# Optimization experiments

Measured on AMD Instinct MI355X. Metric: run time of the kernel, lower is better.

The kernel has to match this reference:

```python
import jax, jax.numpy as jnp
import numpy as np

B, S, D, H = 2, 2048, 1024, 16
DK = D // H


def setup_inputs() -> dict:
    key = jax.random.key(0)
    ks = jax.random.split(key, 8)
    xavier = lambda k, shape: jax.random.uniform(k, shape, jnp.float32, -1.0, 1.0) * np.sqrt(6.0 / (shape[0] + shape[1]))
    return {
        "query": jax.random.normal(ks[0], (B, S, D), jnp.float32),
        "key": jax.random.normal(ks[1], (B, S, D), jnp.float32),
        "value": jax.random.normal(ks[2], (B, S, D), jnp.float32),
        # causal mask: True above the diagonal -> masked out
        "mask": jnp.broadcast_to(jnp.triu(jnp.ones((S, S), bool), k=1), (B, S, S)),
        "w_q": xavier(ks[3], (D, D)),  # torch Linear weight [out, in]
        "w_k": xavier(ks[4], (D, D)),
        "w_v": xavier(ks[5], (D, D)),
        "w_o": xavier(ks[6], (D, D)),
        "b_o": jnp.zeros((D,), jnp.float32),
    }


def reference(query, key, value, mask, w_q, w_k, w_v, w_o, b_o):
    b, sq, d = query.shape
    sk = key.shape[1]
    # projections (torch Linear: x @ W.T)
    Q = (query @ w_q.T).reshape(b, sq, H, DK).transpose(0, 2, 1, 3)  # [B,H,Sq,DK]
    K = (key @ w_k.T).reshape(b, sk, H, DK).transpose(0, 2, 1, 3)
    V = (value @ w_v.T).reshape(b, sk, H, DK).transpose(0, 2, 1, 3)
    scores = jnp.einsum('bhqd,bhkd->bhqk', Q, K) / np.sqrt(DK)
    scores = jnp.where(mask[:, None, :, :], jnp.float32(-1e9), scores)
    attn = jax.nn.softmax(scores, axis=-1)  # dropout is identity in eval
    out = jnp.einsum('bhqk,bhkd->bhqd', attn, V)
    out = out.transpose(0, 2, 1, 3).reshape(b, sq, d)
    return out @ w_o.T + b_o
```

## Files before the change

kernel.cpp:

```cpp
#include <hip/hip_runtime.h>
#include <hip/hip_bf16.h>
#include <stdint.h>


typedef __attribute__((ext_vector_type(4))) float  f32x4;
typedef __attribute__((ext_vector_type(4))) int    i32x4;
typedef __attribute__((ext_vector_type(8))) __bf16 bf16x8;
typedef __attribute__((ext_vector_type(4))) __bf16 bf16x4;
typedef __attribute__((ext_vector_type(2))) __bf16 bf16x2;

#define MFMA16(a, b, c) __builtin_amdgcn_mfma_f32_16x16x32_bf16((a), (b), (c), 0, 0, 0)

__device__ __forceinline__ void async16(const void* g, void* lds) {
  __builtin_amdgcn_global_load_lds(
      (const __attribute__((address_space(1))) uint32_t*)g,
      (__attribute__((address_space(3))) uint32_t*)lds,
      16, 0, 0);
}

__device__ __forceinline__ bf16x8 lds_swz_read(const __bf16* base, int row, int cchunk) {
  const int sw = cchunk ^ (row & 7);
  return *(const bf16x8*)((const char*)base + row * 128 + sw * 16);
}

__global__ void detect_dtype(const uint16_t* __restrict__ w, int* __restrict__ flag) {
  __shared__ int s;
  if (threadIdx.x == 0) s = 0;
  __syncthreads();
  int big = 0;
  for (int i = threadIdx.x; i < 8192; i += 256) {
    uint32_t u = ((uint32_t)w[i]) << 16;
    float f;
    __builtin_memcpy(&f, &u, 4);
    if (fabsf(f) > 1.0f) big = 1;
  }
  if (big) atomicOr(&s, 1);
  __syncthreads();
  if (threadIdx.x == 0) *flag = s;
}

struct CvtArgs { const void* src[8]; void* dst[8]; int n[8]; };

__global__ __launch_bounds__(256)
void convert_all(CvtArgs a, const int* __restrict__ flagp) {
  if (*flagp == 0) return;
  const int t = blockIdx.y;
  const int n = a.n[t];
  const int i0 = (blockIdx.x * 256 + threadIdx.x) * 8;
  if (i0 >= n) return;
  const float* s = (const float*)a.src[t];
  __bf16* d = (__bf16*)a.dst[t];
  bf16x8 v;
#pragma unroll
  for (int j = 0; j < 8; ++j) v[j] = (__bf16)s[i0 + j];
  *(bf16x8*)(d + i0) = v;
}

struct GemmArgs {
  const __bf16* A[3];    const __bf16* W[3];
  const __bf16* Acvt[3]; const __bf16* Wcvt[3];
  void* C[3]; float scale[3];
  const __bf16* bias; const __bf16* biascvt;
  const int* flagp; int mode;
};

__global__ __launch_bounds__(256, 3)
void gemm_nt(GemmArgs ga)
{
  constexpr int K = 1024;
  __shared__ __align__(16) __bf16 smem[16384];

  const int id = blockIdx.x + (blockIdx.y << 3) + (blockIdx.z << 8);
  const int mb = (id & 7) * 4 + ((id >> 3) & 3);
  const int rest = id >> 5;
  const int nb = rest & 7;
  const int z = rest >> 3;

  const int f = *ga.flagp;
  const __bf16* __restrict__ A = f ? ga.Acvt[z] : ga.A[z];
  const __bf16* __restrict__ W = f ? ga.Wcvt[z] : ga.W[z];
  void* __restrict__ C = ga.C[z];
  const float scale = ga.scale[z];
  const int mode = ga.mode;

  const int tid = threadIdx.x;
  const int lane = tid & 63;
  const int wave = tid >> 6;
  const int l15 = lane & 15;
  const int quad = lane >> 4;
  const int bm = mb * 128;
  const int bn = nb * 128;
  const int wm = (wave >> 1) * 64;
  const int wn = (wave & 1) * 64;

  auto stage = [&](int kt, int buf) {
    const int k0 = kt * 32;
    __bf16* As = smem + buf * 8192;
    __bf16* Bs = As + 4096;
#pragma unroll
    for (int r = 0; r < 2; ++r) {
      const int chunk = r * 256 + wave * 64 + lane;
      const int row = chunk >> 2, c = chunk & 3;
      async16(A + (size_t)(bm + row) * K + k0 + c * 8, As + (r * 256 + wave * 64) * 8);
      async16(W + (size_t)(bn + row) * K + k0 + c * 8, Bs + (r * 256 + wave * 64) * 8);
    }
  };

  f32x4 acc[4][4];
#pragma unroll
  for (int mi = 0; mi < 4; ++mi)
#pragma unroll
    for (int ni = 0; ni < 4; ++ni) {
      f32x4 zz = {0.f, 0.f, 0.f, 0.f};
      acc[mi][ni] = zz;
    }

  stage(0, 0);
  __syncthreads();

  for (int kt = 0; kt < K / 32; ++kt) {
    const int cur = kt & 1;
    const __bf16* As = smem + cur * 8192;
    const __bf16* Bs = As + 4096;

    bf16x8 af[4];
    bf16x8 bfr[4];
#pragma unroll
    for (int mi = 0; mi < 4; ++mi)
      af[mi] = *(const bf16x8*)(As + (wm + mi * 16 + l15) * 32 + quad * 8);
#pragma unroll
    for (int ni = 0; ni < 4; ++ni)
      bfr[ni] = *(const bf16x8*)(Bs + (wn + ni * 16 + l15) * 32 + quad * 8);

    if (kt + 1 < K / 32) stage(kt + 1, cur ^ 1);

#pragma unroll
    for (int mi = 0; mi < 4; ++mi)
#pragma unroll
      for (int ni = 0; ni < 4; ++ni)
        acc[mi][ni] = MFMA16(af[mi], bfr[ni], acc[mi][ni]);

    __syncthreads();
  }

  float bv[4] = {0.f, 0.f, 0.f, 0.f};
  if (mode == 1) {
    const __bf16* bias = f ? ga.biascvt : ga.bias;
#pragma unroll
    for (int ni = 0; ni < 4; ++ni) bv[ni] = (float)bias[bn + wn + ni * 16 + l15];
  }
  __bf16 (*Cs)[136] = (__bf16(*)[136])smem;

#pragma unroll
  for (int pass = 0; pass < 2; ++pass) {
    __syncthreads();
    if ((wave >> 1) == pass) {
#pragma unroll
      for (int mi = 0; mi < 4; ++mi)
#pragma unroll
        for (int ni = 0; ni < 4; ++ni)
#pragma unroll
          for (int r = 0; r < 4; ++r)
            Cs[mi * 16 + quad * 4 + r][wn + ni * 16 + l15] =
                (__bf16)(acc[mi][ni][r] * scale + bv[ni]);
    }
    __syncthreads();

    if (mode == 0) {
#pragma unroll
      for (int it = 0; it < 4; ++it) {
        const int cid = it * 256 + tid;
        const int off = cid & 7, seg = cid >> 3;
        const int hl = seg & 1, rowl = seg >> 1;
        f32x4 v = *(const f32x4*)(&Cs[rowl][hl * 64 + off * 8]);
        const int m = bm + pass * 64 + rowl;
        const int b = m >> 11, s = m & 2047;
        const int h = (bn >> 6) + hl;
        *(f32x4*)((__bf16*)C + ((size_t)(b * 16 + h) * 2048 + s) * 64 + off * 8) = v;
      }
    } else if (f) {
#pragma unroll
      for (int it = 0; it < 4; ++it) {
        const int cid = it * 256 + tid;
        const int off = cid & 15, rowl = cid >> 4;
        bf16x8 vb = *(const bf16x8*)(&Cs[rowl][off * 8]);
        const int m = bm + pass * 64 + rowl;
        float* dst = (float*)C + (size_t)m * 1024 + bn + off * 8;
        f32x4 lo, hi;
#pragma unroll
        for (int j = 0; j < 4; ++j) { lo[j] = (float)vb[j]; hi[j] = (float)vb[4 + j]; }
        *(f32x4*)dst = lo;
        *(f32x4*)(dst + 4) = hi;
      }
    } else {
#pragma unroll
      for (int it = 0; it < 4; ++it) {
        const int cid = it * 256 + tid;
        const int off = cid & 15, rowl = cid >> 4;
        bf16x8 vb = *(const bf16x8*)(&Cs[rowl][off * 8]);
        const int m = bm + pass * 64 + rowl;
        *(bf16x8*)((__bf16*)C + (size_t)m * 1024 + bn + off * 8) = vb;
      }
    }
  }
}

__global__ __launch_bounds__(256, 4)
void attn(const __bf16* __restrict__ Q,
          const __bf16* __restrict__ Kg,
          const __bf16* __restrict__ Vg,
          __bf16* __restrict__ O)
{
  __shared__ __align__(16) __bf16 Ks[128 * 64];
  __shared__ __align__(16) __bf16 Vts[64][136];

  const int tid = threadIdx.x;
  const int lane = tid & 63;
  const int wave = tid >> 6;
  const int l15 = lane & 15;
  const int quad = lane >> 4;

  const int zb = blockIdx.x;
  const int qt = 31 - (zb >> 5);
  const int bh = zb & 31;
  const int q0 = qt * 64;
  const int nIter = (qt >> 1) + 1;

  const __bf16* Qp = Q + (size_t)bh * 2048 * 64;
  const __bf16* Kp = Kg + (size_t)bh * 2048 * 64;
  const __bf16* Vp = Vg + (size_t)bh * 2048 * 64;

  const int qrow_wl = wave * 16 + l15;

  bf16x8 qf[2];
#pragma unroll
  for (int kc = 0; kc < 2; ++kc)
    qf[kc] = *(const bf16x8*)(Qp + (size_t)(q0 + qrow_wl) * 64 + kc * 32 + quad * 8);

  f32x4 o_[4];
#pragma unroll
  for (int dt = 0; dt < 4; ++dt) {
    f32x4 zz = {0.f, 0.f, 0.f, 0.f};
    o_[dt] = zz;
  }
  float lsum = 0.0f;

  const int krow[4] = { (0 * 256 + tid) >> 3, (1 * 256 + tid) >> 3,
                        (2 * 256 + tid) >> 3, (3 * 256 + tid) >> 3 };
  const int kcol[4] = { ((0 * 256 + tid) & 7) ^ (krow[0] & 7),
                        ((1 * 256 + tid) & 7) ^ (krow[1] & 7),
                        ((2 * 256 + tid) & 7) ^ (krow[2] & 7),
                        ((3 * 256 + tid) & 7) ^ (krow[3] & 7) };

  const int pp4 = tid & 31;
  const int dgg = tid >> 5;
  const int P0 = (((pp4 & 0x18) | ((pp4 & 3) << 1) | ((pp4 >> 2) & 1)) << 2);

  bf16x8 ka0 = *(const bf16x8*)(Kp + (size_t)krow[0] * 64 + kcol[0] * 8);
  bf16x8 ka1 = *(const bf16x8*)(Kp + (size_t)krow[1] * 64 + kcol[1] * 8);
  bf16x8 ka2 = *(const bf16x8*)(Kp + (size_t)krow[2] * 64 + kcol[2] * 8);
  bf16x8 ka3 = *(const bf16x8*)(Kp + (size_t)krow[3] * 64 + kcol[3] * 8);
  bf16x8 va0 = *(const bf16x8*)(Vp + (size_t)(4 * pp4 + 0) * 64 + dgg * 8);
  bf16x8 va1 = *(const bf16x8*)(Vp + (size_t)(4 * pp4 + 1) * 64 + dgg * 8);
  bf16x8 va2 = *(const bf16x8*)(Vp + (size_t)(4 * pp4 + 2) * 64 + dgg * 8);
  bf16x8 va3 = *(const bf16x8*)(Vp + (size_t)(4 * pp4 + 3) * 64 + dgg * 8);

  for (int t = 0; t < nIter; ++t) {
    *(bf16x8*)((char*)Ks + (0 * 256 + tid) * 16) = ka0;
    *(bf16x8*)((char*)Ks + (1 * 256 + tid) * 16) = ka1;
    *(bf16x8*)((char*)Ks + (2 * 256 + tid) * 16) = ka2;
    *(bf16x8*)((char*)Ks + (3 * 256 + tid) * 16) = ka3;
#pragma unroll
    for (int j = 0; j < 8; ++j) {
      bf16x4 w = { va0[j], va1[j], va2[j], va3[j] };
      *(bf16x4*)(&Vts[dgg * 8 + j][P0]) = w;
    }
    __syncthreads();

    bf16x8 kn0 = ka0, kn1 = ka1, kn2 = ka2, kn3 = ka3;
    bf16x8 vn0 = va0, vn1 = va1, vn2 = va2, vn3 = va3;
    if (t + 1 < nIter) {
      const int k1 = (t + 1) * 128;
      kn0 = *(const bf16x8*)(Kp + (size_t)(k1 + krow[0]) * 64 + kcol[0] * 8);
      kn1 = *(const bf16x8*)(Kp + (size_t)(k1 + krow[1]) * 64 + kcol[1] * 8);
      kn2 = *(const bf16x8*)(Kp + (size_t)(k1 + krow[2]) * 64 + kcol[2] * 8);
      kn3 = *(const bf16x8*)(Kp + (size_t)(k1 + krow[3]) * 64 + kcol[3] * 8);
      vn0 = *(const bf16x8*)(Vp + (size_t)(k1 + 4 * pp4 + 0) * 64 + dgg * 8);
      vn1 = *(const bf16x8*)(Vp + (size_t)(k1 + 4 * pp4 + 1) * 64 + dgg * 8);
      vn2 = *(const bf16x8*)(Vp + (size_t)(k1 + 4 * pp4 + 2) * 64 + dgg * 8);
      vn3 = *(const bf16x8*)(Vp + (size_t)(k1 + 4 * pp4 + 3) * 64 + dgg * 8);
    }

    f32x4 st[8];
#pragma unroll
    for (int nt = 0; nt < 8; ++nt) {
      f32x4 zz = {0.f, 0.f, 0.f, 0.f};
      st[nt] = zz;
    }
    __builtin_amdgcn_s_setprio(1);
#pragma unroll
    for (int kc = 0; kc < 2; ++kc)
#pragma unroll
      for (int nt = 0; nt < 8; ++nt) {
        bf16x8 kf = lds_swz_read(Ks, nt * 16 + l15, kc * 4 + quad);
        st[nt] = MFMA16(kf, qf[kc], st[nt]);
      }
    __builtin_amdgcn_s_setprio(0);

    if (t == (qt >> 1)) {
      const int k0 = t * 128;
#pragma unroll
      for (int nt = 0; nt < 8; ++nt)
#pragma unroll
        for (int r = 0; r < 4; ++r)
          if (k0 + nt * 16 + quad * 4 + r > q0 + qrow_wl) st[nt][r] = -1e30f;
    }

    bf16x8 pf[4];
#pragma unroll
    for (int nt = 0; nt < 8; ++nt)
#pragma unroll
      for (int r = 0; r < 4; ++r) {
        const float pv = __builtin_amdgcn_exp2f(st[nt][r]);
        lsum += pv;
        pf[nt >> 1][(nt & 1) * 4 + r] = (__bf16)pv;
      }

    __builtin_amdgcn_s_setprio(1);
#pragma unroll
    for (int kc = 0; kc < 4; ++kc)
#pragma unroll
      for (int dt = 0; dt < 4; ++dt) {
        bf16x8 vf = *(const bf16x8*)(&Vts[dt * 16 + l15][kc * 32 + quad * 8]);
        o_[dt] = MFMA16(vf, pf[kc], o_[dt]);
      }
    __builtin_amdgcn_s_setprio(0);

    __syncthreads();
    ka0 = kn0; ka1 = kn1; ka2 = kn2; ka3 = kn3;
    va0 = vn0; va1 = vn1; va2 = vn2; va3 = vn3;
  }

  lsum += __shfl_xor(lsum, 16, 64);
  lsum += __shfl_xor(lsum, 32, 64);

  __bf16 (*Ot)[72] = (__bf16(*)[72])&Vts[0][0];
  const float inv_l = 1.0f / lsum;
#pragma unroll
  for (int dt = 0; dt < 4; ++dt)
#pragma unroll
    for (int r = 0; r < 4; r += 2) {
      bf16x2 pr = { (__bf16)(o_[dt][r] * inv_l),
                    (__bf16)(o_[dt][r + 1] * inv_l) };
      *(bf16x2*)(&Ot[qrow_wl][dt * 16 + quad * 4 + r]) = pr;
    }
  __syncthreads();

  const int b = bh >> 4, h = bh & 15;
#pragma unroll
  for (int t = 0; t < 2; ++t) {
    const int i = t * 256 + tid;
    const int row = i >> 3, c = i & 7;
    f32x4 v = *(const f32x4*)(&Ot[row][c * 8]);
    *(f32x4*)(O + (size_t)(b * 2048 + q0 + row) * 1024 + h * 64 + c * 8) = v;
  }
}

extern "C" void kernel_launch(void* const* d_in, const int* in_sizes, int n_in,
                              void* d_out, int out_size, void* d_ws, size_t ws_size,
                              hipStream_t stream) {
  char* ws = (char*)d_ws;
  int* flag = (int*)ws;
  __bf16* Xc0 = (__bf16*)(ws + (1u << 20));
  __bf16* Xc1 = (__bf16*)(ws + (9u << 20));
  __bf16* Xc2 = (__bf16*)(ws + (17u << 20));
  __bf16* Wc0 = (__bf16*)(ws + (25u << 20));
  __bf16* Wc1 = (__bf16*)(ws + (27u << 20));
  __bf16* Wc2 = (__bf16*)(ws + (29u << 20));
  __bf16* Wc3 = (__bf16*)(ws + (31u << 20));
  __bf16* bc  = (__bf16*)(ws + (33u << 20));
  __bf16* Qw  = (__bf16*)(ws + (34u << 20));
  __bf16* Kw  = (__bf16*)(ws + (42u << 20));
  __bf16* Vw  = (__bf16*)(ws + (50u << 20));
  __bf16* Aw  = (__bf16*)(ws + (58u << 20));

  detect_dtype<<<1, 256, 0, stream>>>((const uint16_t*)d_in[4], flag);

  CvtArgs ca;
  ca.src[0] = d_in[0]; ca.dst[0] = Xc0; ca.n[0] = 4194304;
  ca.src[1] = d_in[1]; ca.dst[1] = Xc1; ca.n[1] = 4194304;
  ca.src[2] = d_in[2]; ca.dst[2] = Xc2; ca.n[2] = 4194304;
  ca.src[3] = d_in[4]; ca.dst[3] = Wc0; ca.n[3] = 1048576;
  ca.src[4] = d_in[5]; ca.dst[4] = Wc1; ca.n[4] = 1048576;
  ca.src[5] = d_in[6]; ca.dst[5] = Wc2; ca.n[5] = 1048576;
  ca.src[6] = d_in[7]; ca.dst[6] = Wc3; ca.n[6] = 1048576;
  ca.src[7] = d_in[8]; ca.dst[7] = bc;  ca.n[7] = 1024;
  convert_all<<<dim3(2048, 8), 256, 0, stream>>>(ca, flag);

  GemmArgs g0;
  g0.A[0] = (const __bf16*)d_in[0]; g0.Acvt[0] = Xc0;
  g0.A[1] = (const __bf16*)d_in[1]; g0.Acvt[1] = Xc1;
  g0.A[2] = (const __bf16*)d_in[2]; g0.Acvt[2] = Xc2;
  g0.W[0] = (const __bf16*)d_in[4]; g0.Wcvt[0] = Wc0;
  g0.W[1] = (const __bf16*)d_in[5]; g0.Wcvt[1] = Wc1;
  g0.W[2] = (const __bf16*)d_in[6]; g0.Wcvt[2] = Wc2;
  g0.C[0] = Qw; g0.scale[0] = 0.18033688f;
  g0.C[1] = Kw; g0.scale[1] = 1.0f;
  g0.C[2] = Vw; g0.scale[2] = 1.0f;
  g0.bias = nullptr; g0.biascvt = nullptr; g0.flagp = flag; g0.mode = 0;
  gemm_nt<<<dim3(8, 32, 3), 256, 0, stream>>>(g0);

  attn<<<dim3(1024), 256, 0, stream>>>(Qw, Kw, Vw, Aw);

  GemmArgs g1;
  g1.A[0] = Aw; g1.Acvt[0] = Aw;
  g1.A[1] = nullptr; g1.Acvt[1] = nullptr;
  g1.A[2] = nullptr; g1.Acvt[2] = nullptr;
  g1.W[0] = (const __bf16*)d_in[7]; g1.Wcvt[0] = Wc3;
  g1.W[1] = nullptr; g1.Wcvt[1] = nullptr;
  g1.W[2] = nullptr; g1.Wcvt[2] = nullptr;
  g1.C[0] = d_out; g1.scale[0] = 1.0f;
  g1.C[1] = nullptr; g1.scale[1] = 0.f;
  g1.C[2] = nullptr; g1.scale[2] = 0.f;
  g1.bias = (const __bf16*)d_in[8]; g1.biascvt = bc;
  g1.flagp = flag; g1.mode = 1;
  gemm_nt<<<dim3(8, 32, 1), 256, 0, stream>>>(g1);
}
```

Before: 233.0 us.

## Shrink GEMM M-tile to 64 rows, split row-sum accumulators in attention

The projection GEMM moves from 128x128 to 64x128 tiles, which doubles the block count. Each wave now computes a 32x64 sub-tile, the epilogue runs in a single pass, and the block-to-tile swizzle is remapped. The aim is better CU occupancy and load balance on the small output GEMM, which previously launched only 256 blocks. In exchange, the A-operand reuse per loaded W tile is lower, so global traffic goes up. In attention, the softmax row sum is split into four independent accumulators to shorten the dependency chain, and launch bounds drop from 4 to 3 waves per EU, which may change register allocation.

New measurement: 232.7 us. No clear change (-0.1%).

```diff
diff --git a/kernel.cpp b/kernel.cpp
--- a/kernel.cpp
+++ b/kernel.cpp
@@ -4,7 +4,6 @@
 
 
 typedef __attribute__((ext_vector_type(4))) float  f32x4;
-typedef __attribute__((ext_vector_type(4))) int    i32x4;
 typedef __attribute__((ext_vector_type(8))) __bf16 bf16x8;
 typedef __attribute__((ext_vector_type(4))) __bf16 bf16x4;
 typedef __attribute__((ext_vector_type(2))) __bf16 bf16x2;
@@ -65,16 +64,16 @@
 };
 
 __global__ __launch_bounds__(256, 3)
-void gemm_nt(GemmArgs ga)
+void gemm_nt64(GemmArgs ga)
 {
   constexpr int K = 1024;
-  __shared__ __align__(16) __bf16 smem[16384];
-
-  const int id = blockIdx.x + (blockIdx.y << 3) + (blockIdx.z << 8);
-  const int mb = (id & 7) * 4 + ((id >> 3) & 3);
-  const int rest = id >> 5;
-  const int nb = rest & 7;
-  const int z = rest >> 3;
+  constexpr int NT = K / 32;
+  __shared__ __align__(16) __bf16 smem[12288];
+
+  const int id = blockIdx.x + (blockIdx.y << 3);
+  const int mb = (id & 7) * 8 + ((id >> 3) & 7);
+  const int nb = id >> 6;
+  const int z = blockIdx.z;
 
   const int f = *ga.flagp;
   const __bf16* __restrict__ A = f ? ga.Acvt[z] : ga.A[z];
@@ -88,27 +87,30 @@
   const int wave = tid >> 6;
   const int l15 = lane & 15;
   const int quad = lane >> 4;
-  const int bm = mb * 128;
+  const int bm = mb * 64;
   const int bn = nb * 128;
-  const int wm = (wave >> 1) * 64;
+  const int wm = (wave >> 1) * 32;
   const int wn = (wave & 1) * 64;
 
   auto stage = [&](int kt, int buf) {
     const int k0 = kt * 32;
-    __bf16* As = smem + buf * 8192;
-    __bf16* Bs = As + 4096;
+    __bf16* As = smem + buf * 6144;
+    __bf16* Bs = As + 2048;
+    {
+      const int row = tid >> 2, c = tid & 3;
+      async16(A + (size_t)(bm + row) * K + k0 + c * 8, As + (wave * 64) * 8);
+    }
 #pragma unroll
     for (int r = 0; r < 2; ++r) {
-      const int chunk = r * 256 + wave * 64 + lane;
+      const int chunk = r * 256 + tid;
       const int row = chunk >> 2, c = chunk & 3;
-      async16(A + (size_t)(bm + row) * K + k0 + c * 8, As + (r * 256 + wave * 64) * 8);
       async16(W + (size_t)(bn + row) * K + k0 + c * 8, Bs + (r * 256 + wave * 64) * 8);
     }
   };
 
-  f32x4 acc[4][4];
-#pragma unroll
-  for (int mi = 0; mi < 4; ++mi)
+  f32x4 acc[2][4];
+#pragma unroll
+  for (int mi = 0; mi < 2; ++mi)
 #pragma unroll
     for (int ni = 0; ni < 4; ++ni) {
       f32x4 zz = {0.f, 0.f, 0.f, 0.f};
@@ -118,24 +120,24 @@
   stage(0, 0);
   __syncthreads();
 
-  for (int kt = 0; kt < K / 32; ++kt) {
+  for (int kt = 0; kt < NT; ++kt) {
     const int cur = kt & 1;
-    const __bf16* As = smem + cur * 8192;
-    const __bf16* Bs = As + 4096;
-
-    bf16x8 af[4];
+    const __bf16* As = smem + cur * 6144;
+    const __bf16* Bs = As + 2048;
+
+    bf16x8 af[2];
     bf16x8 bfr[4];
 #pragma unroll
-    for (int mi = 0; mi < 4; ++mi)
+    for (int mi = 0; mi < 2; ++mi)
       af[mi] = *(const bf16x8*)(As + (wm + mi * 16 + l15) * 32 + quad * 8);
 #pragma unroll
     for (int ni = 0; ni < 4; ++ni)
       bfr[ni] = *(const bf16x8*)(Bs + (wn + ni * 16 + l15) * 32 + quad * 8);
 
-    if (kt + 1 < K / 32) stage(kt + 1, cur ^ 1);
-
-#pragma unroll
-    for (int mi = 0; mi < 4; ++mi)
+    if (kt + 1 < NT) stage(kt + 1, cur ^ 1);
+
+#pragma unroll
+    for (int mi = 0; mi < 2; ++mi)
 #pragma unroll
       for (int ni = 0; ni < 4; ++ni)
         acc[mi][ni] = MFMA16(af[mi], bfr[ni], acc[mi][ni]);
@@ -149,63 +151,55 @@
 #pragma unroll
     for (int ni = 0; ni < 4; ++ni) bv[ni] = (float)bias[bn + wn + ni * 16 + l15];
   }
+
   __bf16 (*Cs)[136] = (__bf16(*)[136])smem;
-
-#pragma unroll
-  for (int pass = 0; pass < 2; ++pass) {
-    __syncthreads();
-    if ((wave >> 1) == pass) {
-#pragma unroll
-      for (int mi = 0; mi < 4; ++mi)
-#pragma unroll
-        for (int ni = 0; ni < 4; ++ni)
-#pragma unroll
-          for (int r = 0; r < 4; ++r)
-            Cs[mi * 16 + quad * 4 + r][wn + ni * 16 + l15] =
-                (__bf16)(acc[mi][ni][r] * scale + bv[ni]);
-    }
-    __syncthreads();
-
-    if (mode == 0) {
-#pragma unroll
-      for (int it = 0; it < 4; ++it) {
-        const int cid = it * 256 + tid;
-        const int off = cid & 7, seg = cid >> 3;
-        const int hl = seg & 1, rowl = seg >> 1;
-        f32x4 v = *(const f32x4*)(&Cs[rowl][hl * 64 + off * 8]);
-        const int m = bm + pass * 64 + rowl;
-        const int b = m >> 11, s = m & 2047;
-        const int h = (bn >> 6) + hl;
-        *(f32x4*)((__bf16*)C + ((size_t)(b * 16 + h) * 2048 + s) * 64 + off * 8) = v;
-      }
-    } else if (f) {
-#pragma unroll
-      for (int it = 0; it < 4; ++it) {
-        const int cid = it * 256 + tid;
-        const int off = cid & 15, rowl = cid >> 4;
-        bf16x8 vb = *(const bf16x8*)(&Cs[rowl][off * 8]);
-        const int m = bm + pass * 64 + rowl;
-        float* dst = (float*)C + (size_t)m * 1024 + bn + off * 8;
-        f32x4 lo, hi;
-#pragma unroll
-        for (int j = 0; j < 4; ++j) { lo[j] = (float)vb[j]; hi[j] = (float)vb[4 + j]; }
-        *(f32x4*)dst = lo;
-        *(f32x4*)(dst + 4) = hi;
-      }
-    } else {
-#pragma unroll
-      for (int it = 0; it < 4; ++it) {
-        const int cid = it * 256 + tid;
-        const int off = cid & 15, rowl = cid >> 4;
-        bf16x8 vb = *(const bf16x8*)(&Cs[rowl][off * 8]);
-        const int m = bm + pass * 64 + rowl;
-        *(bf16x8*)((__bf16*)C + (size_t)m * 1024 + bn + off * 8) = vb;
-      }
-    }
-  }
-}
-
-__global__ __launch_bounds__(256, 4)
+#pragma unroll
+  for (int mi = 0; mi < 2; ++mi)
+#pragma unroll
+    for (int ni = 0; ni < 4; ++ni)
+#pragma unroll
+      for (int r = 0; r < 4; ++r)
+        Cs[wm + mi * 16 + quad * 4 + r][wn + ni * 16 + l15] =
+            (__bf16)(acc[mi][ni][r] * scale + bv[ni]);
+  __syncthreads();
+
+  if (mode == 0) {
+#pragma unroll
+    for (int it = 0; it < 4; ++it) {
+      const int cid = it * 256 + tid;
+      const int off = cid & 7, seg = cid >> 3;
+      const int hl = seg & 1, rowl = seg >> 1;
+      f32x4 v = *(const f32x4*)(&Cs[rowl][hl * 64 + off * 8]);
+      const int m = bm + rowl;
+      const int b = m >> 11, s = m & 2047;
+      const int h = (bn >> 6) + hl;
+      *(f32x4*)((__bf16*)C + ((size_t)(b * 16 + h) * 2048 + s) * 64 + off * 8) = v;
+    }
+  } else if (f) {
+#pragma unroll
+    for (int it = 0; it < 4; ++it) {
+      const int cid = it * 256 + tid;
+      const int off = cid & 15, rowl = cid >> 4;
+      bf16x8 vb = *(const bf16x8*)(&Cs[rowl][off * 8]);
+      float* dst = (float*)C + (size_t)(bm + rowl) * 1024 + bn + off * 8;
+      f32x4 lo, hi;
+#pragma unroll
+      for (int j = 0; j < 4; ++j) { lo[j] = (float)vb[j]; hi[j] = (float)vb[4 + j]; }
+      *(f32x4*)dst = lo;
+      *(f32x4*)(dst + 4) = hi;
+    }
+  } else {
+#pragma unroll
+    for (int it = 0; it < 4; ++it) {
+      const int cid = it * 256 + tid;
+      const int off = cid & 15, rowl = cid >> 4;
+      bf16x8 vb = *(const bf16x8*)(&Cs[rowl][off * 8]);
+      *(bf16x8*)((__bf16*)C + (size_t)(bm + rowl) * 1024 + bn + off * 8) = vb;
+    }
+  }
+}
+
+__global__ __launch_bounds__(256, 3)
 void attn(const __bf16* __restrict__ Q,
           const __bf16* __restrict__ Kg,
           const __bf16* __restrict__ Vg,
@@ -243,23 +237,21 @@
     f32x4 zz = {0.f, 0.f, 0.f, 0.f};
     o_[dt] = zz;
   }
-  float lsum = 0.0f;
-
-  const int krow[4] = { (0 * 256 + tid) >> 3, (1 * 256 + tid) >> 3,
-                        (2 * 256 + tid) >> 3, (3 * 256 + tid) >> 3 };
-  const int kcol[4] = { ((0 * 256 + tid) & 7) ^ (krow[0] & 7),
-                        ((1 * 256 + tid) & 7) ^ (krow[1] & 7),
-                        ((2 * 256 + tid) & 7) ^ (krow[2] & 7),
-                        ((3 * 256 + tid) & 7) ^ (krow[3] & 7) };
+  f32x4 ls4 = {0.f, 0.f, 0.f, 0.f};
+
+  const int krow0 = (0 * 256 + tid) >> 3, kc0 = ((0 * 256 + tid) & 7) ^ (krow0 & 7);
+  const int krow1 = (1 * 256 + tid) >> 3, kc1 = ((1 * 256 + tid) & 7) ^ (krow1 & 7);
+  const int krow2 = (2 * 256 + tid) >> 3, kc2 = ((2 * 256 + tid) & 7) ^ (krow2 & 7);
+  const int krow3 = (3 * 256 + tid) >> 3, kc3 = ((3 * 256 + tid) & 7) ^ (krow3 & 7);
 
   const int pp4 = tid & 31;
   const int dgg = tid >> 5;
   const int P0 = (((pp4 & 0x18) | ((pp4 & 3) << 1) | ((pp4 >> 2) & 1)) << 2);
 
-  bf16x8 ka0 = *(const bf16x8*)(Kp + (size_t)krow[0] * 64 + kcol[0] * 8);
-  bf16x8 ka1 = *(const bf16x8*)(Kp + (size_t)krow[1] * 64 + kcol[1] * 8);
-  bf16x8 ka2 = *(const bf16x8*)(Kp + (size_t)krow[2] * 64 + kcol[2] * 8);
-  bf16x8 ka3 = *(const bf16x8*)(Kp + (size_t)krow[3] * 64 + kcol[3] * 8);
+  bf16x8 ka0 = *(const bf16x8*)(Kp + (size_t)krow0 * 64 + kc0 * 8);
+  bf16x8 ka1 = *(const bf16x8*)(Kp + (size_t)krow1 * 64 + kc1 * 8);
+  bf16x8 ka2 = *(const bf16x8*)(Kp + (size_t)krow2 * 64 + kc2 * 8);
+  bf16x8 ka3 = *(const bf16x8*)(Kp + (size_t)krow3 * 64 + kc3 * 8);
   bf16x8 va0 = *(const bf16x8*)(Vp + (size_t)(4 * pp4 + 0) * 64 + dgg * 8);
   bf16x8 va1 = *(const bf16x8*)(Vp + (size_t)(4 * pp4 + 1) * 64 + dgg * 8);
   bf16x8 va2 = *(const bf16x8*)(Vp + (size_t)(4 * pp4 + 2) * 64 + dgg * 8);
@@ -281,10 +273,10 @@
     bf16x8 vn0 = va0, vn1 = va1, vn2 = va2, vn3 = va3;
     if (t + 1 < nIter) {
       const int k1 = (t + 1) * 128;
-      kn0 = *(const bf16x8*)(Kp + (size_t)(k1 + krow[0]) * 64 + kcol[0] * 8);
-      kn1 = *(const bf16x8*)(Kp + (size_t)(k1 + krow[1]) * 64 + kcol[1] * 8);
-      kn2 = *(const bf16x8*)(Kp + (size_t)(k1 + krow[2]) * 64 + kcol[2] * 8);
-      kn3 = *(const bf16x8*)(Kp + (size_t)(k1 + krow[3]) * 64 + kcol[3] * 8);
+      kn0 = *(const bf16x8*)(Kp + (size_t)(k1 + krow0) * 64 + kc0 * 8);
+      kn1 = *(const bf16x8*)(Kp + (size_t)(k1 + krow1) * 64 + kc1 * 8);
+      kn2 = *(const bf16x8*)(Kp + (size_t)(k1 + krow2) * 64 + kc2 * 8);
+      kn3 = *(const bf16x8*)(Kp + (size_t)(k1 + krow3) * 64 + kc3 * 8);
       vn0 = *(const bf16x8*)(Vp + (size_t)(k1 + 4 * pp4 + 0) * 64 + dgg * 8);
       vn1 = *(const bf16x8*)(Vp + (size_t)(k1 + 4 * pp4 + 1) * 64 + dgg * 8);
       vn2 = *(const bf16x8*)(Vp + (size_t)(k1 + 4 * pp4 + 2) * 64 + dgg * 8);
@@ -322,7 +314,7 @@
 #pragma unroll
       for (int r = 0; r < 4; ++r) {
         const float pv = __builtin_amdgcn_exp2f(st[nt][r]);
-        lsum += pv;
+        ls4[r] += pv;
         pf[nt >> 1][(nt & 1) * 4 + r] = (__bf16)pv;
       }
 
@@ -341,6 +333,7 @@
     va0 = vn0; va1 = vn1; va2 = vn2; va3 = vn3;
   }
 
+  float lsum = (ls4[0] + ls4[1]) + (ls4[2] + ls4[3]);
   lsum += __shfl_xor(lsum, 16, 64);
   lsum += __shfl_xor(lsum, 32, 64);
 
@@ -408,7 +401,7 @@
   g0.C[1] = Kw; g0.scale[1] = 1.0f;
   g0.C[2] = Vw; g0.scale[2] = 1.0f;
   g0.bias = nullptr; g0.biascvt = nullptr; g0.flagp = flag; g0.mode = 0;
-  gemm_nt<<<dim3(8, 32, 3), 256, 0, stream>>>(g0);
+  gemm_nt64<<<dim3(8, 64, 3), 256, 0, stream>>>(g0);
 
   attn<<<dim3(1024), 256, 0, stream>>>(Qw, Kw, Vw, Aw);
 
@@ -424,5 +417,5 @@
   g1.C[2] = nullptr; g1.scale[2] = 0.f;
   g1.bias = (const __bf16*)d_in[8]; g1.biascvt = bc;
   g1.flagp = flag; g1.mode = 1;
-  gemm_nt<<<dim3(8, 32, 1), 256, 0, stream>>>(g1);
-}
+  gemm_nt64<<<dim3(8, 64, 1), 256, 0, stream>>>(g1);
+}
```
